# Kernel optimization log

Hardware: AMD Instinct MI355X
Metric: run time of the kernel (lower is better)

Reference implementation:

```python
import jax, jax.numpy as jnp
import numpy as np
from itertools import product

N = 200000      # occupied fine voxels
G = 256         # grid extent per axis
C0, C1 = 32, 64 # nPlanes
EPS = 1e-4      # BatchNormBlock eps


def _enc(p):
    return (p[:, 0].astype(np.int64) * G + p[:, 1]) * G + p[:, 2]


def _lookup(q, keys):
    # keys: sorted encoded positions; returns index into position array, sentinel=len(keys) if absent
    n = keys.shape[0]
    valid = ((q >= 0) & (q < G)).all(1)
    qe = _enc(np.clip(q, 0, G - 1))
    i = np.searchsorted(keys, qe)
    ic = np.clip(i, 0, n - 1)
    found = valid & (keys[ic] == qe)
    return np.where(found, ic, n).astype(np.int32)


def _build_geometry():
    rng = np.random.default_rng(0)
    lin = np.sort(rng.choice(G ** 3, size=N, replace=False))
    pos = np.stack(np.unravel_index(lin, (G, G, G)), -1).astype(np.int64)  # [N,3], enc(pos)==lin sorted
    keys = lin
    off27 = np.array(list(product((-1, 0, 1), repeat=3)), dtype=np.int64)
    nbr_fine = np.stack([_lookup(pos + o, keys) for o in off27])  # [27,N]
    # Convolution.calculate_grid: even positions among pos+{-1,0}^3, min>=0, unique, then /2
    f8 = np.array(list(product((-1, 0), repeat=3)), dtype=np.int64)
    cand = (pos[:, None, :] + f8[None]).reshape(-1, 3)
    cand = cand[cand.min(1) >= 0]
    cand = cand[(cand % 2 == 0).all(1)]
    cand = np.unique(cand, axis=0)
    cpos = cand // 2                       # [M,3] coarse coords
    ckeys = _enc(cpos)                     # lexsorted rows -> sorted keys
    off2 = np.array([[(i >> 2) & 1, (i >> 1) & 1, i & 1] for i in range(8)], dtype=np.int64)
    down_idx = np.stack([_lookup(2 * cpos + o, keys) for o in off2])  # [8,M] into fine feats

    def _lookup_c(q):
        n = ckeys.shape[0]
        valid = ((q >= 0) & (q < G)).all(1)
        qe = _enc(np.clip(q, 0, G - 1))
        i = np.searchsorted(ckeys, qe)
        ic = np.clip(i, 0, n - 1)
        found = valid & (ckeys[ic] == qe)
        return np.where(found, ic, n).astype(np.int32)

    nbr_coarse = np.stack([_lookup_c(cpos + o) for o in off27])  # [27,M]
    up_cidx = _lookup_c(pos // 2)  # [N], always found (coverage guaranteed by calculate_grid)
    up_k = ((pos[:, 0] % 2) * 4 + (pos[:, 1] % 2) * 2 + (pos[:, 2] % 2)).astype(np.int32)
    return nbr_fine, nbr_coarse, down_idx, up_cidx, up_k


def setup_inputs() -> dict:
    nbr_fine, nbr_coarse, down_idx, up_cidx, up_k = _build_geometry()
    key = jax.random.key(0)
    ks = jax.random.split(key, 8)

    def w(k, shape, fan_in):
        return jax.random.normal(k, shape, jnp.float32) * (1.0 / np.sqrt(fan_in))

    return dict(
        feat=jax.random.normal(ks[0], (N, C0), jnp.float32),
        w_sub1=w(ks[1], (27, C0, C0), 27 * C0),
        w_down=w(ks[2], (8, C0, C1), 8 * C0),
        w_sub2=w(ks[3], (27, C1, C1), 27 * C1),
        w_up=w(ks[4], (8, C1, C0), 8 * C1),
        w_sub3=w(ks[5], (27, 2 * C0, C0), 27 * 2 * C0),
        g1=jnp.ones(C0), b1=jnp.zeros(C0),
        g2=jnp.ones(C0), b2=jnp.zeros(C0),
        g3=jnp.ones(C1), b3=jnp.zeros(C1),
        g4=jnp.ones(C1), b4=jnp.zeros(C1),
        g5=jnp.ones(2 * C0), b5=jnp.zeros(2 * C0),
        nbr_fine=jnp.asarray(nbr_fine), nbr_coarse=jnp.asarray(nbr_coarse),
        down_idx=jnp.asarray(down_idx), up_cidx=jnp.asarray(up_cidx),
        up_k=jnp.asarray(up_k),
    )


def _bn_relu(x, g, b):
    # BatchNormBlock (training-mode batch stats over concatenated voxels) + ReLUBlock
    mu = x.mean(0)
    var = x.var(0)
    return jax.nn.relu(g * (x - mu) * jax.lax.rsqrt(var + EPS) + b)


def _sparse_conv(feat, nbr, W):
    # gather-GEMM-accumulate: feat [P,Cin], nbr [K,M] (sentinel P -> zero), W [K,Cin,Cout]
    fpad = jnp.concatenate([feat, jnp.zeros((1, feat.shape[1]), feat.dtype)], 0)

    def body(acc, kw):
        idx, w = kw
        return acc + fpad[idx] @ w, None

    acc0 = jnp.zeros((nbr.shape[1], W.shape[2]), feat.dtype)
    out, _ = jax.lax.scan(body, acc0, (nbr, W))
    return out


def _sparse_deconv(cfeat, up_cidx, up_k, W):
    # stride-2 transpose conv: each fine voxel reads its unique coarse parent with kernel tap up_k
    g = cfeat[up_cidx]  # [N,Cin]
    out = jnp.zeros((g.shape[0], W.shape[2]), cfeat.dtype)
    for k in range(8):
        out = out + jnp.where(up_k == k, 1.0, 0.0)[:, None] * (g @ W[k])
    return out


def reference(feat, w_sub1, w_down, w_sub2, w_up, w_sub3,
              g1, b1, g2, b2, g3, b3, g4, b4, g5, b5,
              nbr_fine, nbr_coarse, down_idx, up_cidx, up_k):
    # block(32->32): BN -> ReLU -> SubmanifoldSparseConv 3x3x3
    x = _sparse_conv(_bn_relu(feat, g1, b1), nbr_fine, w_sub1)
    skip = x  # ConcatFeat
    # BN -> ReLU -> Convolution 2x2x2 (downsample 32->64)
    xc = _sparse_conv(_bn_relu(x, g2, b2), down_idx, w_down)
    # inner level block(64->64)
    xc = _sparse_conv(_bn_relu(xc, g3, b3), nbr_coarse, w_sub2)
    # BN -> ReLU -> DeConvolution 2x2x2 (upsample 64->32)
    xf = _sparse_deconv(_bn_relu(xc, g4, b4), up_cidx, up_k, w_up)
    # JoinFeat: concat(skip, upsampled)
    x = jnp.concatenate([skip, xf], -1)
    # block(64->32)
    x = _sparse_conv(_bn_relu(x, g5, b5), nbr_fine, w_sub3)
    return x
```

## Files before the change

### kernel.cpp

```cpp
#include <hip/hip_runtime.h>


#define EPS 1e-4f

typedef __attribute__((ext_vector_type(8))) short short8;
typedef __attribute__((ext_vector_type(4))) float f32x4;

__device__ __forceinline__ unsigned short f2bf(float f) {
    union { float f; unsigned int u; } v; v.f = f;
    unsigned int r = v.u + 0x7fffu + ((v.u >> 16) & 1u);
    return (unsigned short)(r >> 16);
}

__global__ void zero_kernel(float* p, long n) {
    long i = (long)blockIdx.x * 256 + threadIdx.x;
    if (i < n) p[i] = 0.f;
}

template <int C>
__global__ __launch_bounds__(256) void bn_stats(const float* __restrict__ x,
                                                int rows, int stride,
                                                float* __restrict__ stats) {
    const int tid = threadIdx.x;
    const int c = tid & (C - 1);
    const int g = tid / C;
    const int GR = 256 / C;
    float s = 0.f, s2 = 0.f;
    for (int r = blockIdx.x * GR + g; r < rows; r += gridDim.x * GR) {
        float v = x[(size_t)r * stride + c];
        s += v; s2 += v * v;
    }
    __shared__ float sh[2][256];
    sh[0][tid] = s; sh[1][tid] = s2;
    __syncthreads();
    for (int off = 128; off >= C; off >>= 1) {
        if (tid < off) { sh[0][tid] += sh[0][tid + off]; sh[1][tid] += sh[1][tid + off]; }
        __syncthreads();
    }
    if (tid < C) {
        atomicAdd(&stats[c], sh[0][tid]);
        atomicAdd(&stats[C + c], sh[1][tid]);
    }
}

template <int C, int CSPLIT>
__global__ __launch_bounds__(256) void bn_norm_relu_bf16(
    const float* __restrict__ x, int rows, int stride,
    const float* __restrict__ stA, const float* __restrict__ stB,
    const float* __restrict__ gamma, const float* __restrict__ beta,
    unsigned short* __restrict__ y) {
    constexpr int TPR = C / 8;
    int gid = blockIdx.x * 256 + threadIdx.x;
    int r = gid / TPR, t = gid % TPR;
    if (r > rows) return;
    short8 o8;
    if (r == rows) {
        for (int j = 0; j < 8; ++j) o8[j] = 0;
    } else {
        const float inv_n = 1.0f / (float)rows;
        const float* xr = x + (size_t)r * stride + t * 8;
        float4 v0 = *(const float4*)(xr);
        float4 v1 = *(const float4*)(xr + 4);
        float vv[8] = {v0.x, v0.y, v0.z, v0.w, v1.x, v1.y, v1.z, v1.w};
#pragma unroll
        for (int j = 0; j < 8; ++j) {
            int c = t * 8 + j;
            const float* st = (c < CSPLIT) ? stA : stB;
            int cc = (c < CSPLIT) ? c : c - CSPLIT;
            int cs = (c < CSPLIT) ? CSPLIT : (C - CSPLIT);
            float mu = st[cc] * inv_n;
            float var = st[cs + cc] * inv_n - mu * mu;
            float sc = gamma[c] * rsqrtf(var + EPS);
            float shf = beta[c] - mu * sc;
            float ov = fmaxf(0.f, fmaf(vv[j], sc, shf));
            o8[j] = (short)f2bf(ov);
        }
    }
    *(short8*)(y + (size_t)r * C + t * 8) = o8;
}

__device__ __forceinline__ void wt_seg(const float* W, unsigned short* WT,
                                       int id, int CIN, int COUT) {
    int r = id % (CIN * COUT);
    int t = id / (CIN * COUT);
    int co = r / CIN;
    int ci = r % CIN;
    int ksub = CIN >> 5;
    int nt = co >> 4, l15 = co & 15;
    int kf = (ksub > 1) ? (ci >> 5) : 0;
    int qq = (ci >> 3) & 3;
    int e  = ci & 7;
    int off = ((nt * ksub + kf) * 64 + (qq * 16 + l15)) * 8 + e;
    WT[(size_t)t * CIN * COUT + off] = f2bf(W[(size_t)t * CIN * COUT + ci * COUT + co]);
}
__global__ __launch_bounds__(256) void wt_transpose_all(
    const float* w1, const float* wd, const float* w2, const float* w3,
    const float* wu, unsigned short* o1, unsigned short* od,
    unsigned short* o2, unsigned short* o3, unsigned short* ou) {
    int id = blockIdx.x * 256 + threadIdx.x;
    if (id < 27648) { wt_seg(w1, o1, id, 32, 32); return; }
    id -= 27648;
    if (id < 16384) { wt_seg(wd, od, id, 32, 64); return; }
    id -= 16384;
    if (id < 110592) { wt_seg(w2, o2, id, 64, 64); return; }
    id -= 110592;
    if (id < 55296) { wt_seg(w3, o3, id, 64, 32); return; }
    id -= 55296;
    if (id < 16384) { wt_seg(wu, ou, id, 64, 32); return; }
}

__global__ __launch_bounds__(256) void build_rb_up(
    const int* __restrict__ up_cidx, const int* __restrict__ up_k,
    int rows, int cap, int2* __restrict__ rb, int* __restrict__ cnt) {
    const int s = blockIdx.y;
    const int lane = threadIdx.x & 63;
    const int wave = threadIdx.x >> 6;
    const long wbase = (long)blockIdx.x * 1024 + wave * 256;

    unsigned long long masks[4];
    int cs[4], ok[4], tot[4], wtotal = 0;
#pragma unroll
    for (int c = 0; c < 4; ++c) {
        long i = wbase + c * 64 + lane;
        int seg = (i < rows) ? up_k[i] : -1;
        cs[c] = (i < rows) ? up_cidx[i] : 0;
        ok[c] = (seg == s);
        masks[c] = __ballot(ok[c]);
        tot[c] = __popcll(masks[c]);
        wtotal += tot[c];
    }
    __shared__ int sh[5];
    if (lane == 0) sh[wave] = wtotal;
    __syncthreads();
    if (threadIdx.x == 0) {
        int t = sh[0] + sh[1] + sh[2] + sh[3];
        sh[4] = t ? atomicAdd(&cnt[s * 32], t) : 0;
    }
    __syncthreads();
    int base = sh[4];
    for (int w = 0; w < wave; ++w) base += sh[w];
#pragma unroll
    for (int c = 0; c < 4; ++c) {
        if (ok[c]) {
            int rank = __popcll(masks[c] & ((1ull << lane) - 1ull));
            int j = base + rank;
            if (j < cap)
                rb[(size_t)s * cap + j] = make_int2((int)(wbase + c * 64 + lane), cs[c]);
        }
        base += tot[c];
    }
}


template <int CIN, int COT, int NTAP, int MT>
__global__ __launch_bounds__(256) void conv_dense(
    const unsigned short* __restrict__ fpad,
    const int* __restrict__ nbr,
    const unsigned short* __restrict__ WT,
    float* __restrict__ out,
    float* __restrict__ stats,
    int rows, int P, int out_stride) {
    constexpr int N_SUB = COT / 16;
    constexpr int K_SUB = CIN / 32;
    constexpr int MH = MT / 2;
    const int tid = threadIdx.x;
    const int wave = tid >> 6;
    const int lane = tid & 63;
    const int q = lane >> 4;
    const int l15 = lane & 15;
    const int m0 = blockIdx.x * (64 * MT) + wave * (16 * MT);

    int mrow[MT], mok[MT];
#pragma unroll
    for (int mt = 0; mt < MT; ++mt) {
        int m = m0 + mt * 16 + l15;
        mok[mt] = (m < rows);
        mrow[mt] = mok[mt] ? m : 0;
    }

    f32x4 acc[MT][N_SUB];
#pragma unroll
    for (int mt = 0; mt < MT; ++mt)
#pragma unroll
        for (int nt = 0; nt < N_SUB; ++nt) acc[mt][nt] = (f32x4){0.f, 0.f, 0.f, 0.f};

    short8 aLo[MH][K_SUB], aHi[MH][K_SUB];
    short8 b[N_SUB][K_SUB];
    int idxN[MT];

    auto load_idx = [&](int k) {
#pragma unroll
        for (int mt = 0; mt < MT; ++mt)
            idxN[mt] = mok[mt] ? nbr[(size_t)k * rows + mrow[mt]] : P;
    };
    auto gather_half = [&](short8 (&a)[MH][K_SUB], int hoff) {
#pragma unroll
        for (int h = 0; h < MH; ++h) {
            const unsigned short* ap = fpad + (size_t)idxN[hoff + h] * CIN + q * 8;
#pragma unroll
            for (int kf = 0; kf < K_SUB; ++kf)
                a[h][kf] = *(const short8*)(ap + kf * 32);
        }
    };
    auto gather_half0 = [&](short8 (&a)[MH][K_SUB], int hoff, int k0) {
#pragma unroll
        for (int h = 0; h < MH; ++h) {
            int idx = mok[hoff + h] ? nbr[(size_t)k0 * rows + mrow[hoff + h]] : P;
            const unsigned short* ap = fpad + (size_t)idx * CIN + q * 8;
#pragma unroll
            for (int kf = 0; kf < K_SUB; ++kf)
                a[h][kf] = *(const short8*)(ap + kf * 32);
        }
    };
    auto load_b = [&](int k) {
        const unsigned short* Wk = WT + (size_t)k * COT * CIN;
#pragma unroll
        for (int nt = 0; nt < N_SUB; ++nt)
#pragma unroll
            for (int kf = 0; kf < K_SUB; ++kf)
                b[nt][kf] = *(const short8*)(Wk + ((nt * K_SUB + kf) * 64 + lane) * 8);
    };
    auto mfma_half = [&](short8 (&a)[MH][K_SUB], int hoff) {
#pragma unroll
        for (int h = 0; h < MH; ++h)
#pragma unroll
            for (int nt = 0; nt < N_SUB; ++nt)
#pragma unroll
                for (int kf = 0; kf < K_SUB; ++kf)
                    acc[hoff + h][nt] = __builtin_amdgcn_mfma_f32_16x16x32_bf16(
                        a[h][kf], b[nt][kf], acc[hoff + h][nt], 0, 0, 0);
    };

    gather_half0(aLo, 0, 0);
    gather_half0(aHi, MH, 0);
    load_b(0);
    if (NTAP > 1) load_idx(1);

#pragma unroll
    for (int k = 0; k < NTAP; ++k) {
        const bool more = (k + 1 < NTAP);
        mfma_half(aLo, 0);
        if (more) gather_half(aLo, 0);
        mfma_half(aHi, MH);
        if (more) {
            load_b(k + 1);
            gather_half(aHi, MH);
            if (k + 2 < NTAP) load_idx(k + 2);
        }
    }

#pragma unroll
    for (int mt = 0; mt < MT; ++mt)
#pragma unroll
        for (int i = 0; i < 4; ++i) {
            int row = m0 + mt * 16 + q * 4 + i;
            if (row < rows) {
#pragma unroll
                for (int nt = 0; nt < N_SUB; ++nt)
                    out[(size_t)row * out_stride + nt * 16 + l15] = acc[mt][nt][i];
            }
        }

    if (stats) {
        __shared__ float ssum[COT], ssq[COT];
        for (int i = tid; i < 2 * COT; i += 256)
            (i < COT ? ssum[i] : ssq[i - COT]) = 0.f;
        __syncthreads();
#pragma unroll
        for (int nt = 0; nt < N_SUB; ++nt) {
            float s = 0.f, s2 = 0.f;
#pragma unroll
            for (int mt = 0; mt < MT; ++mt)
#pragma unroll
                for (int i = 0; i < 4; ++i) {
                    float v = acc[mt][nt][i];
                    s += v; s2 += v * v;
                }
            s += __shfl_xor(s, 16);  s += __shfl_xor(s, 32);
            s2 += __shfl_xor(s2, 16); s2 += __shfl_xor(s2, 32);
            if (q == 0) {
                atomicAdd(&ssum[nt * 16 + l15], s);
                atomicAdd(&ssq[nt * 16 + l15], s2);
            }
        }
        __syncthreads();
        if (tid < COT) {
            atomicAdd(&stats[tid], ssum[tid]);
            atomicAdd(&stats[COT + tid], ssq[tid]);
        }
    }
}

template <int CIN, int COT, bool ATOMIC>
__global__ __launch_bounds__(256) void conv_sparse(
    const unsigned short* __restrict__ fpad,
    const int2* __restrict__ rb,
    const int* __restrict__ cnt,
    const unsigned short* __restrict__ WT,
    float* __restrict__ out,
    float* __restrict__ stats,
    int cap, int kskip, int P, int out_stride) {
    constexpr int N_SUB = COT / 16;
    constexpr int K_SUB = CIN / 32;
    const int tap = blockIdx.y;
    int n = cnt[tap * 32];
    n = n < cap ? n : cap;
    const int nbx = gridDim.x;
    const int step = (nbx >> 3) | 1;
    const int px = (int)((blockIdx.x + (unsigned)tap * step) % (unsigned)nbx);
    const int base0 = px * 128;
    if (base0 >= n) return;
    const int k = tap + (tap >= kskip ? 1 : 0);
    const int tid = threadIdx.x;
    const int wave = tid >> 6;
    const int lane = tid & 63;
    const int q = lane >> 4;
    const int l15 = lane & 15;
    const int base = base0 + wave * 32;
    const int2* seg = rb + (size_t)tap * cap;

    f32x4 acc[2][N_SUB];
#pragma unroll
    for (int mt = 0; mt < 2; ++mt)
#pragma unroll
        for (int nt = 0; nt < N_SUB; ++nt) acc[mt][nt] = (f32x4){0.f, 0.f, 0.f, 0.f};

    short8 a[2][K_SUB], b[N_SUB][K_SUB];
#pragma unroll
    for (int mt = 0; mt < 2; ++mt) {
        int j = base + mt * 16 + l15;
        int src = (j < n) ? seg[j].y : P;
#pragma unroll
        for (int kf = 0; kf < K_SUB; ++kf)
            a[mt][kf] = *(const short8*)(fpad + (size_t)src * CIN + kf * 32 + q * 8);
    }
    const unsigned short* Wk = WT + (size_t)k * COT * CIN;
#pragma unroll
    for (int nt = 0; nt < N_SUB; ++nt)
#pragma unroll
        for (int kf = 0; kf < K_SUB; ++kf)
            b[nt][kf] = *(const short8*)(Wk + ((nt * K_SUB + kf) * 64 + lane) * 8);
#pragma unroll
    for (int mt = 0; mt < 2; ++mt)
#pragma unroll
        for (int nt = 0; nt < N_SUB; ++nt)
#pragma unroll
            for (int kf = 0; kf < K_SUB; ++kf)
                acc[mt][nt] = __builtin_amdgcn_mfma_f32_16x16x32_bf16(
                    a[mt][kf], b[nt][kf], acc[mt][nt], 0, 0, 0);

#pragma unroll
    for (int mt = 0; mt < 2; ++mt)
#pragma unroll
        for (int i = 0; i < 4; ++i) {
            int j = base + mt * 16 + q * 4 + i;
            if (j < n) {
                int row = seg[j].x;
                float* o = out + (size_t)row * out_stride + l15;
#pragma unroll
                for (int nt = 0; nt < N_SUB; ++nt) {
                    if (ATOMIC) atomicAdd(o + nt * 16, acc[mt][nt][i]);
                    else        o[nt * 16] = acc[mt][nt][i];
                }
            }
        }

    if (!ATOMIC && stats) {
        __shared__ float ssum[COT], ssq[COT];
        for (int i = tid; i < 2 * COT; i += 256)
            (i < COT ? ssum[i] : ssq[i - COT]) = 0.f;
        __syncthreads();
#pragma unroll
        for (int nt = 0; nt < N_SUB; ++nt) {
            float s = 0.f, s2 = 0.f;
#pragma unroll
            for (int mt = 0; mt < 2; ++mt)
#pragma unroll
                for (int i = 0; i < 4; ++i) {
                    float v = acc[mt][nt][i];
                    s += v; s2 += v * v;
                }
            s += __shfl_xor(s, 16);  s += __shfl_xor(s, 32);
            s2 += __shfl_xor(s2, 16); s2 += __shfl_xor(s2, 32);
            if (q == 0) {
                atomicAdd(&ssum[nt * 16 + l15], s);
                atomicAdd(&ssq[nt * 16 + l15], s2);
            }
        }
        __syncthreads();
        if (tid < COT) {
            atomicAdd(&stats[tid], ssum[tid]);
            atomicAdd(&stats[COT + tid], ssq[tid]);
        }
    }
}

static inline int ceil_div(long a, long b) { return (int)((a + b - 1) / b); }

extern "C" void kernel_launch(void* const* d_in, const int* in_sizes, int n_in,
                              void* d_out, int out_size, void* d_ws, size_t ws_size,
                              hipStream_t stream) {
    const float* feat   = (const float*)d_in[0];
    const float* w_sub1 = (const float*)d_in[1];
    const float* w_down = (const float*)d_in[2];
    const float* w_sub2 = (const float*)d_in[3];
    const float* w_up   = (const float*)d_in[4];
    const float* w_sub3 = (const float*)d_in[5];
    const float* g1 = (const float*)d_in[6],  *b1 = (const float*)d_in[7];
    const float* g2 = (const float*)d_in[8],  *b2 = (const float*)d_in[9];
    const float* g3 = (const float*)d_in[10], *b3 = (const float*)d_in[11];
    const float* g4 = (const float*)d_in[12], *b4 = (const float*)d_in[13];
    const float* g5 = (const float*)d_in[14], *b5 = (const float*)d_in[15];
    const int* nbr_fine   = (const int*)d_in[16];
    const int* nbr_coarse = (const int*)d_in[17];
    const int* down_idx   = (const int*)d_in[18];
    const int* up_cidx    = (const int*)d_in[19];
    const int* up_k       = (const int*)d_in[20];

    const int N = in_sizes[0] / 32;
    const int M = in_sizes[17] / 27;
    const size_t maxr = (size_t)((N > M ? N : M) + 1);

    const int cap_u = 32768;

    char* ws = (char*)d_ws;
    size_t off = 0;
    auto alloc = [&](size_t bytes) { void* p = ws + off; off += (bytes + 255) & ~(size_t)255; return p; };
    float* stats = (float*)alloc(768 * sizeof(float));
    int*   cnts  = (int*)alloc(1024 * sizeof(int));
    const size_t zero_words = off / 4;
    float* D  = (float*)alloc((size_t)N * 64 * sizeof(float));
    float* Cf = (float*)alloc((size_t)M * 64 * sizeof(float));
    unsigned short* FA = (unsigned short*)alloc(maxr * 64 * 2);
    unsigned short* FB = (unsigned short*)alloc(maxr * 64 * 2);
    int2* rb_up = (int2*)alloc((size_t)8 * cap_u * sizeof(int2));
    unsigned short* w1t = (unsigned short*)alloc(27 * 32 * 32 * 2);
    unsigned short* wdt = (unsigned short*)alloc(8 * 32 * 64 * 2);
    unsigned short* w2t = (unsigned short*)alloc(27 * 64 * 64 * 2);
    unsigned short* w3t = (unsigned short*)alloc(27 * 64 * 32 * 2);
    unsigned short* wupT = (unsigned short*)alloc(8 * 64 * 32 * 2);

    float* st0 = stats + 0 * 128;
    float* st1 = stats + 1 * 128;
    float* st2 = stats + 2 * 128;
    float* st3 = stats + 3 * 128;
    float* st4 = stats + 4 * 128;
    int* cnt_up = cnts;

    zero_kernel<<<ceil_div((long)zero_words, 256), 256, 0, stream>>>(stats, (long)zero_words);
    wt_transpose_all<<<ceil_div(226304, 256), 256, 0, stream>>>(
        w_sub1, w_down, w_sub2, w_sub3, w_up, w1t, wdt, w2t, w3t, wupT);
    build_rb_up<<<dim3(ceil_div(N, 1024), 8), 256, 0, stream>>>(
        up_cidx, up_k, N, cap_u, rb_up, cnt_up);

    bn_stats<32><<<256, 256, 0, stream>>>(feat, N, 32, st0);
    bn_norm_relu_bf16<32, 32><<<ceil_div((long)(N + 1) * 4, 256), 256, 0, stream>>>(
        feat, N, 32, st0, st0, g1, b1, FA);
    conv_dense<32, 32, 27, 2><<<ceil_div(N, 128), 256, 0, stream>>>(
        FA, nbr_fine, w1t, D, st1, N, N, 64);
    bn_norm_relu_bf16<32, 32><<<ceil_div((long)(N + 1) * 4, 256), 256, 0, stream>>>(
        D, N, 64, st1, st1, g2, b2, FB);
    conv_dense<32, 64, 8, 2><<<ceil_div(M, 128), 256, 0, stream>>>(
        FB, down_idx, wdt, Cf, st2, M, N, 64);
    bn_norm_relu_bf16<64, 64><<<ceil_div((long)(M + 1) * 8, 256), 256, 0, stream>>>(
        Cf, M, 64, st2, st2, g3, b3, FA);
    conv_dense<64, 64, 27, 2><<<ceil_div(M, 128), 256, 0, stream>>>(
        FA, nbr_coarse, w2t, Cf, st3, M, M, 64);
    bn_norm_relu_bf16<64, 64><<<ceil_div((long)(M + 1) * 8, 256), 256, 0, stream>>>(
        Cf, M, 64, st3, st3, g4, b4, FB);
    conv_sparse<64, 32, false><<<dim3(cap_u / 128, 8), 256, 0, stream>>>(
        FB, rb_up, cnt_up, wupT, D + 32, st4, cap_u, 99, M, 64);
    bn_norm_relu_bf16<64, 32><<<ceil_div((long)(N + 1) * 8, 256), 256, 0, stream>>>(
        D, N, 64, st1, st4, g5, b5, FA);
    conv_dense<64, 32, 27, 2><<<ceil_div(N, 128), 256, 0, stream>>>(
        FA, nbr_fine, w3t, (float*)d_out, nullptr, N, N, 32);
}
```

Measured before the change: 564.5 us.

## Stage conv weights in LDS via async global_load_lds with double-buffered tap phases

Dense sparse-conv kernels now stage a group of weight taps into shared memory with asynchronous global-to-LDS loads, double-buffered across phases, and read B fragments from LDS instead of global memory each tap. The row tile per wave also goes from 2 to 4 sub-tiles, so each block covers 256 rows and reuses the weights across more rows. This cuts redundant global and L2 weight traffic. The cost is extra block barriers, LDS use and register pressure from the larger accumulator tile, which may lower occupancy. Staging the next phase right after the barrier could race with slow waves still reading that buffer.

```diff
diff --git a/kernel.cpp b/kernel.cpp
--- a/kernel.cpp
+++ b/kernel.cpp
@@ -152,7 +152,7 @@
 }
 
 
-template <int CIN, int COT, int NTAP, int MT>
+template <int CIN, int COT, int NTAP, int MT, int TPP>
 __global__ __launch_bounds__(256) void conv_dense(
     const unsigned short* __restrict__ fpad,
     const int* __restrict__ nbr,
@@ -163,6 +163,10 @@
     constexpr int N_SUB = COT / 16;
     constexpr int K_SUB = CIN / 32;
     constexpr int MH = MT / 2;
+    constexpr int TAP_SH = COT * CIN;
+    constexpr int PHASES = (NTAP + TPP - 1) / TPP;
+    constexpr int NBUF = (PHASES > 1) ? 2 : 1;
+    __shared__ unsigned short ldsB[NBUF][TPP * TAP_SH];
     const int tid = threadIdx.x;
     const int wave = tid >> 6;
     const int lane = tid & 63;
@@ -188,6 +192,26 @@
     short8 b[N_SUB][K_SUB];
     int idxN[MT];
 
+    auto stage_phase = [&](int ph, int buf) {
+        const int t0 = ph * TPP;
+        const int cnt = (t0 + TPP <= NTAP) ? TPP : (NTAP - t0);
+        const unsigned short* src = WT + (size_t)t0 * TAP_SH;
+        const int tot = cnt * TAP_SH / 512;
+        for (int j = wave; j < tot; j += 4) {
+            __builtin_amdgcn_global_load_lds(
+                (const __attribute__((address_space(1))) void*)(src + j * 512 + lane * 8),
+                (__attribute__((address_space(3))) void*)(&ldsB[buf][j * 512]),
+                16, 0, 0);
+        }
+    };
+    auto load_b_lds = [&](int buf, int kk) {
+#pragma unroll
+        for (int nt = 0; nt < N_SUB; ++nt)
+#pragma unroll
+            for (int kf = 0; kf < K_SUB; ++kf)
+                b[nt][kf] = *(const short8*)(
+                    &ldsB[buf][kk * TAP_SH + ((nt * K_SUB + kf) * 64 + lane) * 8]);
+    };
     auto load_idx = [&](int k) {
 #pragma unroll
         for (int mt = 0; mt < MT; ++mt)
@@ -212,14 +236,6 @@
                 a[h][kf] = *(const short8*)(ap + kf * 32);
         }
     };
-    auto load_b = [&](int k) {
-        const unsigned short* Wk = WT + (size_t)k * COT * CIN;
-#pragma unroll
-        for (int nt = 0; nt < N_SUB; ++nt)
-#pragma unroll
-            for (int kf = 0; kf < K_SUB; ++kf)
-                b[nt][kf] = *(const short8*)(Wk + ((nt * K_SUB + kf) * 64 + lane) * 8);
-    };
     auto mfma_half = [&](short8 (&a)[MH][K_SUB], int hoff) {
 #pragma unroll
         for (int h = 0; h < MH; ++h)
@@ -231,22 +247,31 @@
                         a[h][kf], b[nt][kf], acc[hoff + h][nt], 0, 0, 0);
     };
 
+    stage_phase(0, 0);
+    load_idx(0);
     gather_half0(aLo, 0, 0);
     gather_half0(aHi, MH, 0);
-    load_b(0);
     if (NTAP > 1) load_idx(1);
+    __syncthreads();
 
 #pragma unroll
     for (int k = 0; k < NTAP; ++k) {
+        constexpr int NB1 = NBUF - 1;
+        const int ph = k / TPP;
+        const int cur = ph & NB1;
         const bool more = (k + 1 < NTAP);
+        load_b_lds(cur, k - ph * TPP);
+        if (k % TPP == 0 && ph + 1 < PHASES)
+            stage_phase(ph + 1, (ph + 1) & NB1);
         mfma_half(aLo, 0);
         if (more) gather_half(aLo, 0);
         mfma_half(aHi, MH);
         if (more) {
-            load_b(k + 1);
             gather_half(aHi, MH);
             if (k + 2 < NTAP) load_idx(k + 2);
         }
+        if ((k + 1) % TPP == 0 && (k + 1) < NTAP)
+            __syncthreads();
     }
 
 #pragma unroll
@@ -456,15 +481,15 @@
     bn_stats<32><<<256, 256, 0, stream>>>(feat, N, 32, st0);
     bn_norm_relu_bf16<32, 32><<<ceil_div((long)(N + 1) * 4, 256), 256, 0, stream>>>(
         feat, N, 32, st0, st0, g1, b1, FA);
-    conv_dense<32, 32, 27, 2><<<ceil_div(N, 128), 256, 0, stream>>>(
+    conv_dense<32, 32, 27, 4, 4><<<ceil_div(N, 256), 256, 0, stream>>>(
         FA, nbr_fine, w1t, D, st1, N, N, 64);
     bn_norm_relu_bf16<32, 32><<<ceil_div((long)(N + 1) * 4, 256), 256, 0, stream>>>(
         D, N, 64, st1, st1, g2, b2, FB);
-    conv_dense<32, 64, 8, 2><<<ceil_div(M, 128), 256, 0, stream>>>(
+    conv_dense<32, 64, 8, 4, 4><<<ceil_div(M, 256), 256, 0, stream>>>(
         FB, down_idx, wdt, Cf, st2, M, N, 64);
     bn_norm_relu_bf16<64, 64><<<ceil_div((long)(M + 1) * 8, 256), 256, 0, stream>>>(
         Cf, M, 64, st2, st2, g3, b3, FA);
-    conv_dense<64, 64, 27, 2><<<ceil_div(M, 128), 256, 0, stream>>>(
+    conv_dense<64, 64, 27, 4, 2><<<ceil_div(M, 256), 256, 0, stream>>>(
         FA, nbr_coarse, w2t, Cf, st3, M, M, 64);
     bn_norm_relu_bf16<64, 64><<<ceil_div((long)(M + 1) * 8, 256), 256, 0, stream>>>(
         Cf, M, 64, st3, st3, g4, b4, FB);
@@ -472,6 +497,6 @@
         FB, rb_up, cnt_up, wupT, D + 32, st4, cap_u, 99, M, 64);
     bn_norm_relu_bf16<64, 32><<<ceil_div((long)(N + 1) * 8, 256), 256, 0, stream>>>(
         D, N, 64, st1, st4, g5, b5, FA);
-    conv_dense<64, 32, 27, 2><<<ceil_div(N, 128), 256, 0, stream>>>(
+    conv_dense<64, 32, 27, 4, 4><<<ceil_div(N, 256), 256, 0, stream>>>(
         FA, nbr_fine, w3t, (float*)d_out, nullptr, N, N, 32);
 }
```

Result: no change. 574.2 us (+1.7%).
